# Performance work log

Measured on AMD Instinct MI355X. Metric: run time of the kernel, lower is better.

Reference implementation:

```python
import jax, jax.numpy as jnp
import numpy as np
from jax import lax

B, S, N, F = 64, 512, 30, 1
H, HD = 2, 8              # n_heads, head_dim (gat_hidden=16)
GH = H * HD               # gat_hidden
P = 64                    # projection_dim
LH = 64                   # lstm_hidden
ALPHA = 0.2


def setup_inputs() -> dict:
    key = jax.random.key(0)
    ks = jax.random.split(key, 16)
    x = jax.random.normal(ks[0], (B, S, N, F), dtype=jnp.float32)
    adj = jax.random.randint(ks[1], (N, N), 0, 2).astype(jnp.float32)
    adj = jnp.maximum(adj, jnp.eye(N, dtype=jnp.float32))  # self-loops, no empty rows
    sc = 0.1
    W_gat = sc * jax.random.normal(ks[2], (H, F, HD), dtype=jnp.float32)
    a_src = sc * jax.random.normal(ks[3], (H, HD), dtype=jnp.float32)
    a_dst = sc * jax.random.normal(ks[4], (H, HD), dtype=jnp.float32)
    W_proj = sc * jax.random.normal(ks[5], (N * GH, P), dtype=jnp.float32)
    b_proj = jnp.zeros((P,), dtype=jnp.float32)
    W_ih0 = sc * jax.random.normal(ks[6], (4 * LH, P), dtype=jnp.float32)
    W_hh0 = sc * jax.random.normal(ks[7], (4 * LH, LH), dtype=jnp.float32)
    b_ih0 = jnp.zeros((4 * LH,), dtype=jnp.float32)
    b_hh0 = jnp.zeros((4 * LH,), dtype=jnp.float32)
    W_ih1 = sc * jax.random.normal(ks[8], (4 * LH, LH), dtype=jnp.float32)
    W_hh1 = sc * jax.random.normal(ks[9], (4 * LH, LH), dtype=jnp.float32)
    b_ih1 = jnp.zeros((4 * LH,), dtype=jnp.float32)
    b_hh1 = jnp.zeros((4 * LH,), dtype=jnp.float32)
    W_out = sc * jax.random.normal(ks[10], (LH, N * F), dtype=jnp.float32)
    b_out = jnp.zeros((N * F,), dtype=jnp.float32)
    return dict(x=x, adj=adj, W_gat=W_gat, a_src=a_src, a_dst=a_dst,
                W_proj=W_proj, b_proj=b_proj,
                W_ih0=W_ih0, W_hh0=W_hh0, b_ih0=b_ih0, b_hh0=b_hh0,
                W_ih1=W_ih1, W_hh1=W_hh1, b_ih1=b_ih1, b_hh1=b_hh1,
                W_out=W_out, b_out=b_out)


def _gat(x_flat, adj, W_gat, a_src, a_dst):
    # x_flat: (BS, N, F)
    h = jnp.einsum('bnf,hfd->bhnd', x_flat, W_gat)          # (BS, H, N, HD)
    e_src = jnp.einsum('bhnd,hd->bhn', h, a_src)
    e_dst = jnp.einsum('bhnd,hd->bhn', h, a_dst)
    e = e_src[..., :, None] + e_dst[..., None, :]           # (BS, H, N, N)
    e = jnp.where(e >= 0, e, ALPHA * e)                     # leaky_relu
    e = jnp.where(adj == 0, -jnp.inf, e)
    attn = jax.nn.softmax(e, axis=-1)
    attn = jnp.nan_to_num(attn, nan=0.0)
    out = jnp.einsum('bhij,bhjd->bhid', attn, h)            # (BS, H, N, HD)
    out = jnp.swapaxes(out, 1, 2).reshape(out.shape[0], N, GH)  # head-concat
    out = jnp.where(out > 0, out, jnp.expm1(out))           # elu
    attn_avg = attn.mean(axis=1)                            # (BS, N, N)
    return out, attn_avg


def _lstm_layer(xs, W_ih, W_hh, b_ih, b_hh):
    # xs: (B, S, D) -> (B, S, LH); torch gate order i,f,g,o
    b = xs.shape[0]
    h0 = jnp.zeros((b, LH), xs.dtype)
    c0 = jnp.zeros((b, LH), xs.dtype)

    def step(carry, x_t):
        h, c = carry
        gates = x_t @ W_ih.T + b_ih + h @ W_hh.T + b_hh
        i, f, g, o = jnp.split(gates, 4, axis=-1)
        i, f, o = jax.nn.sigmoid(i), jax.nn.sigmoid(f), jax.nn.sigmoid(o)
        g = jnp.tanh(g)
        c = f * c + i * g
        h = o * jnp.tanh(c)
        return (h, c), h

    (_, _), hs = lax.scan(step, (h0, c0), jnp.swapaxes(xs, 0, 1))
    return jnp.swapaxes(hs, 0, 1)


def reference(x, adj, W_gat, a_src, a_dst, W_proj, b_proj,
              W_ih0, W_hh0, b_ih0, b_hh0, W_ih1, W_hh1, b_ih1, b_hh1,
              W_out, b_out):
    b, s, n, f = x.shape
    x_flat = x.reshape(b * s, n, f)
    gat_out, attn = _gat(x_flat, adj, W_gat, a_src, a_dst)   # (BS,N,GH),(BS,N,N)
    gat_seq = gat_out.reshape(b, s, n * GH)
    gat_seq = jax.nn.relu(gat_seq @ W_proj + b_proj)         # (B,S,P)
    h1 = _lstm_layer(gat_seq, W_ih0, W_hh0, b_ih0, b_hh0)
    h2 = _lstm_layer(h1, W_ih1, W_hh1, b_ih1, b_hh1)
    recon = h2 @ W_out + b_out                               # (B,S,N*F)
    attn_last = attn.reshape(b, s, n, n)[:, -1]              # (B,N,N)
    return recon, attn_last
```

## Files before the change

### kernel.cpp

```cpp
#include <hip/hip_runtime.h>
#include <math.h>

#define BS_TOT 32768
#define NN 30
#define HHD 8
#define GHH 16
#define LHH 64
#define SSS 512
#define BBB 64
#define RECON_SIZE (BBB*SSS*NN)

__device__ __forceinline__ float fsigmoid(float x) {
    return 1.f / (1.f + __expf(-x));
}
__device__ __forceinline__ float ftanh(float x) {
    float ax = fabsf(x);
    float e = __expf(-2.f * ax);
    float r = (1.f - e) / (1.f + e);
    return copysignf(r, x);
}

#define NB 16
__global__ __launch_bounds__(256) void gat_proj_kernel(
    const float* __restrict__ x, const float* __restrict__ adj,
    const float* __restrict__ W_gat, const float* __restrict__ a_src,
    const float* __restrict__ a_dst, const float* __restrict__ W_proj,
    const float* __restrict__ b_proj, float* __restrict__ gat_seq,
    float* __restrict__ attn_out)
{
    __shared__ __align__(16) float gat[NB][480];
    __shared__ __align__(16) float wchunk[96*64];
    __shared__ float x_s[NB][32];
    __shared__ unsigned adjbits[32];

    const int t = threadIdx.x;
    const int bs_base = blockIdx.x * NB;

    for (int rep = 0; rep < 2; ++rep) {
        int idx = rep*256 + t;
        int bl = idx >> 5, j = idx & 31;
        if (j < NN) x_s[bl][j] = x[(bs_base + bl)*NN + j];
    }
    if (t < NN) {
        unsigned bits = 0;
        for (int j = 0; j < NN; ++j)
            if (adj[t*NN + j] != 0.0f) bits |= (1u << j);
        adjbits[t] = bits;
    }
    __syncthreads();

    const int wave = t >> 6, lane = t & 63;
    const int h = lane >> 5, i = lane & 31;
    const bool act = (i < NN);

    float wg[HHD];
    float s_h = 0.f, t_h = 0.f;
    #pragma unroll
    for (int d = 0; d < HHD; ++d) {
        float w = W_gat[h*HHD + d];
        wg[d] = w;
        s_h += w * a_src[h*HHD + d];
        t_h += w * a_dst[h*HHD + d];
    }

    for (int r = 0; r < 4; ++r) {
        const int bl = wave*4 + r;
        const int bs = bs_base + bl;
        const unsigned bits = act ? adjbits[i & 31] : 0u;
        const float xi = act ? x_s[bl][i] : 0.f;
        const float esrc = xi * s_h;

        float m = -1e30f;
        for (int j = 0; j < NN; ++j) {
            if (bits & (1u << j)) {
                float e = esrc + x_s[bl][j] * t_h;
                e = (e >= 0.f) ? e : 0.2f * e;
                m = fmaxf(m, e);
            }
        }
        float Z = 0.f, Sx = 0.f;
        for (int j = 0; j < NN; ++j) {
            if (bits & (1u << j)) {
                float e = esrc + x_s[bl][j] * t_h;
                e = (e >= 0.f) ? e : 0.2f * e;
                float p = expf(e - m);
                Z += p;
                Sx += p * x_s[bl][j];
            }
        }
        const float wsum = Sx / Z;

        if (act) {
            float tmp[8];
            #pragma unroll
            for (int d = 0; d < 8; ++d) {
                float v = wsum * wg[d];
                tmp[d] = (v > 0.f) ? v : expm1f(v);
            }
            float4 v0 = make_float4(tmp[0], tmp[1], tmp[2], tmp[3]);
            float4 v1 = make_float4(tmp[4], tmp[5], tmp[6], tmp[7]);
            *(float4*)&gat[bl][i*GHH + h*HHD]     = v0;
            *(float4*)&gat[bl][i*GHH + h*HHD + 4] = v1;
        }

        if ((bs & (SSS-1)) == (SSS-1)) {
            const int b = bs >> 9;
            for (int j = 0; j < NN; ++j) {
                float a = 0.f;
                if (bits & (1u << j)) {
                    float e = esrc + x_s[bl][j] * t_h;
                    e = (e >= 0.f) ? e : 0.2f * e;
                    a = expf(e - m) / Z;
                }
                float ao = __shfl_xor(a, 32, 64);
                if (act && h == 0)
                    attn_out[b*(NN*NN) + i*NN + j] = 0.5f * (a + ao);
            }
        }
    }
    __syncthreads();

    const int p = t & 63, grp = t >> 6;
    float acc0 = 0.f, acc1 = 0.f, acc2 = 0.f, acc3 = 0.f;
    for (int c = 0; c < 5; ++c) {
        #pragma unroll
        for (int rep = 0; rep < 24; ++rep)
            wchunk[rep*256 + t] = W_proj[c*6144 + rep*256 + t];
        __syncthreads();
        for (int kk = 0; kk < 96; kk += 4) {
            float4 g0 = *(const float4*)&gat[grp*4 + 0][c*96 + kk];
            float4 g1 = *(const float4*)&gat[grp*4 + 1][c*96 + kk];
            float4 g2 = *(const float4*)&gat[grp*4 + 2][c*96 + kk];
            float4 g3 = *(const float4*)&gat[grp*4 + 3][c*96 + kk];
            float w0 = wchunk[(kk+0)*64 + p];
            float w1 = wchunk[(kk+1)*64 + p];
            float w2 = wchunk[(kk+2)*64 + p];
            float w3 = wchunk[(kk+3)*64 + p];
            acc0 += g0.x*w0 + g0.y*w1 + g0.z*w2 + g0.w*w3;
            acc1 += g1.x*w0 + g1.y*w1 + g1.z*w2 + g1.w*w3;
            acc2 += g2.x*w0 + g2.y*w1 + g2.z*w2 + g2.w*w3;
            acc3 += g3.x*w0 + g3.y*w1 + g3.z*w2 + g3.w*w3;
        }
        __syncthreads();
    }
    const float bp = b_proj[p];
    gat_seq[(bs_base + grp*4 + 0)*64 + p] = fmaxf(acc0 + bp, 0.f);
    gat_seq[(bs_base + grp*4 + 1)*64 + p] = fmaxf(acc1 + bp, 0.f);
    gat_seq[(bs_base + grp*4 + 2)*64 + p] = fmaxf(acc2 + bp, 0.f);
    gat_seq[(bs_base + grp*4 + 3)*64 + p] = fmaxf(acc3 + bp, 0.f);
}

__global__ __launch_bounds__(256) void xproj_kernel(
    const float* __restrict__ xin,
    const float* __restrict__ W,
    const float* __restrict__ b_ih, const float* __restrict__ b_hh,
    float* __restrict__ gx)
{
    __shared__ __align__(16) float xt[64][64];
    const int t = threadIdx.x;
    const int r0 = blockIdx.x * 64;

    for (int i = t; i < 64*16; i += 256) {
        int r = i >> 4, c4 = (i & 15) << 2;
        *(float4*)&xt[r][c4] = *(const float4*)&xin[(size_t)(r0 + r)*64 + c4];
    }
    float4 w[16];
    #pragma unroll
    for (int i = 0; i < 16; ++i) w[i] = *(const float4*)&W[t*64 + 4*i];
    const float bias = b_ih[t] + b_hh[t];
    __syncthreads();

    for (int r = 0; r < 64; ++r) {
        float a0 = 0.f, a1 = 0.f, a2 = 0.f, a3 = 0.f;
        #pragma unroll
        for (int i = 0; i < 16; ++i) {
            float4 v = *(const float4*)&xt[r][4*i];
            a0 = fmaf(v.x, w[i].x, a0); a1 = fmaf(v.y, w[i].y, a1);
            a2 = fmaf(v.z, w[i].z, a2); a3 = fmaf(v.w, w[i].w, a3);
        }
        gx[(size_t)(r0 + r)*256 + t] = bias + ((a0 + a1) + (a2 + a3));
    }
}

__global__ __launch_bounds__(1024, 1) void lstm_rec_kernel(
    const float* __restrict__ gx,
    const float* __restrict__ W_hh,
    float* __restrict__ h_out)
{
    __shared__ float h_s[64];
    __shared__ float gates[256];

    const int t = threadIdx.x;
    const int b = blockIdx.x;
    const int row = t >> 2, slice = t & 3;
    const int sect = row >> 6;

    const float4 w0 = *(const float4*)&W_hh[row*64 + slice*16 + 0];
    const float4 w1 = *(const float4*)&W_hh[row*64 + slice*16 + 4];
    const float4 w2 = *(const float4*)&W_hh[row*64 + slice*16 + 8];
    const float4 w3 = *(const float4*)&W_hh[row*64 + slice*16 + 12];

    if (t < 64) h_s[t] = 0.f;
    __syncthreads();

    const float* __restrict__ gxb = gx + (size_t)b * SSS * 256;
    float* __restrict__ hrow = h_out + (size_t)b * SSS * 64;

    float c = 0.f;
    float gx_cur = gxb[row];

    for (int tt = 0; tt < SSS; ++tt) {
        float gx_next = (tt + 1 < SSS) ? gxb[(size_t)(tt+1)*256 + row] : 0.f;

        const float4 h0 = *(const float4*)&h_s[slice*16 + 0];
        const float4 h1 = *(const float4*)&h_s[slice*16 + 4];
        const float4 h2 = *(const float4*)&h_s[slice*16 + 8];
        const float4 h3 = *(const float4*)&h_s[slice*16 + 12];

        float a0 = h0.x*w0.x + h0.y*w0.y + h0.z*w0.z + h0.w*w0.w;
        float a1 = h1.x*w1.x + h1.y*w1.y + h1.z*w1.z + h1.w*w1.w;
        float a2 = h2.x*w2.x + h2.y*w2.y + h2.z*w2.z + h2.w*w2.w;
        float a3 = h3.x*w3.x + h3.y*w3.y + h3.z*w3.z + h3.w*w3.w;
        float acc = (a0 + a1) + (a2 + a3);

        acc += __shfl_xor(acc, 1, 64);
        acc += __shfl_xor(acc, 2, 64);
        acc += gx_cur;

        const float a = (sect == 2) ? ftanh(acc) : fsigmoid(acc);
        if (slice == 0) gates[row] = a;
        __syncthreads();

        if (t < 64) {
            float ig = gates[t], fg = gates[64+t], gg = gates[128+t], og = gates[192+t];
            c = fg*c + ig*gg;
            float hv = og * ftanh(c);
            h_s[t] = hv;
            hrow[(size_t)tt*64 + t] = hv;
        }
        gx_cur = gx_next;
        __syncthreads();
    }
}

__global__ __launch_bounds__(256) void recon_kernel(
    const float* __restrict__ h2, const float* __restrict__ W_out,
    const float* __restrict__ b_out, float* __restrict__ out)
{
    __shared__ __align__(16) float hl[8*64];
    const int t = threadIdx.x;
    const int bs_base = blockIdx.x * 8;

    hl[t]       = h2[(size_t)bs_base*64 + t];
    hl[256 + t] = h2[(size_t)bs_base*64 + 256 + t];
    __syncthreads();

    if (t < 240) {
        const int bl = t / 30;
        const int n  = t - bl*30;
        float acc = b_out[n];
        #pragma unroll
        for (int k = 0; k < 64; ++k)
            acc += hl[bl*64 + k] * W_out[k*NN + n];
        out[(size_t)(bs_base + bl)*NN + n] = acc;
    }
}

extern "C" void kernel_launch(void* const* d_in, const int* in_sizes, int n_in,
                              void* d_out, int out_size, void* d_ws, size_t ws_size,
                              hipStream_t stream)
{
    const float* x      = (const float*)d_in[0];
    const float* adj    = (const float*)d_in[1];
    const float* W_gat  = (const float*)d_in[2];
    const float* a_src  = (const float*)d_in[3];
    const float* a_dst  = (const float*)d_in[4];
    const float* W_proj = (const float*)d_in[5];
    const float* b_proj = (const float*)d_in[6];
    const float* W_ih0  = (const float*)d_in[7];
    const float* W_hh0  = (const float*)d_in[8];
    const float* b_ih0  = (const float*)d_in[9];
    const float* b_hh0  = (const float*)d_in[10];
    const float* W_ih1  = (const float*)d_in[11];
    const float* W_hh1  = (const float*)d_in[12];
    const float* b_ih1  = (const float*)d_in[13];
    const float* b_hh1  = (const float*)d_in[14];
    const float* W_out  = (const float*)d_in[15];
    const float* b_out  = (const float*)d_in[16];

    float* out = (float*)d_out;
    float* gat_seq = (float*)d_ws;
    float* h1  = gat_seq + (size_t)BS_TOT*64;
    float* h2  = h1 + (size_t)BS_TOT*64;
    float* gxb = h2 + (size_t)BS_TOT*64;

    hipLaunchKernelGGL(gat_proj_kernel, dim3(BS_TOT/NB), dim3(256), 0, stream,
                       x, adj, W_gat, a_src, a_dst, W_proj, b_proj,
                       gat_seq, out + RECON_SIZE);
    hipLaunchKernelGGL(xproj_kernel, dim3(BS_TOT/64), dim3(256), 0, stream,
                       gat_seq, W_ih0, b_ih0, b_hh0, gxb);
    hipLaunchKernelGGL(lstm_rec_kernel, dim3(BBB), dim3(1024), 0, stream,
                       gxb, W_hh0, h1);
    hipLaunchKernelGGL(xproj_kernel, dim3(BS_TOT/64), dim3(256), 0, stream,
                       h1, W_ih1, b_ih1, b_hh1, gxb);
    hipLaunchKernelGGL(lstm_rec_kernel, dim3(BBB), dim3(1024), 0, stream,
                       gxb, W_hh1, h2);
    hipLaunchKernelGGL(recon_kernel, dim3(BS_TOT/8), dim3(256), 0, stream,
                       h2, W_out, b_out, out);
}
```

Before: 773.3 us.

## Restructure LSTM recurrence to one barrier per step with wave-local gate exchange

The recurrent LSTM kernel drops from 1024 to 512 threads, so each thread now handles half a weight row (32 elements) instead of a quarter. Threads are arranged so all four gates of a hidden unit sit in the same wavefront and are exchanged with shuffles rather than through shared memory. Double-buffering the hidden state removes one of the two block barriers per timestep. Tanh for the g gate is computed through the sigmoid identity, and the weight registers are pinned with empty asm; the cost is more serial FMAs per thread and more register pressure.

```diff
diff --git a/kernel.cpp b/kernel.cpp
--- a/kernel.cpp
+++ b/kernel.cpp
@@ -182,61 +182,88 @@
     }
 }
 
-__global__ __launch_bounds__(1024, 1) void lstm_rec_kernel(
+__global__ __launch_bounds__(512) void lstm_rec_kernel(
     const float* __restrict__ gx,
     const float* __restrict__ W_hh,
     float* __restrict__ h_out)
 {
-    __shared__ float h_s[64];
-    __shared__ float gates[256];
+    __shared__ __align__(16) float h_s[2][64];
 
     const int t = threadIdx.x;
     const int b = blockIdx.x;
-    const int row = t >> 2, slice = t & 3;
-    const int sect = row >> 6;
-
-    const float4 w0 = *(const float4*)&W_hh[row*64 + slice*16 + 0];
-    const float4 w1 = *(const float4*)&W_hh[row*64 + slice*16 + 4];
-    const float4 w2 = *(const float4*)&W_hh[row*64 + slice*16 + 8];
-    const float4 w3 = *(const float4*)&W_hh[row*64 + slice*16 + 12];
-
-    if (t < 64) h_s[t] = 0.f;
-    __syncthreads();
+    const int lane = t & 63;
+    const int jj = lane >> 3, q = (lane >> 1) & 3, s = lane & 1;
+    const int j = (t >> 6) * 8 + jj;
+    const int row = q * 64 + j;
+    const bool qg = (q == 2);
+    const int gbase = (jj << 3);
+
+    float4 w0 = *(const float4*)&W_hh[row*64 + s*32 +  0];
+    float4 w1 = *(const float4*)&W_hh[row*64 + s*32 +  4];
+    float4 w2 = *(const float4*)&W_hh[row*64 + s*32 +  8];
+    float4 w3 = *(const float4*)&W_hh[row*64 + s*32 + 12];
+    float4 w4 = *(const float4*)&W_hh[row*64 + s*32 + 16];
+    float4 w5 = *(const float4*)&W_hh[row*64 + s*32 + 20];
+    float4 w6 = *(const float4*)&W_hh[row*64 + s*32 + 24];
+    float4 w7 = *(const float4*)&W_hh[row*64 + s*32 + 28];
+#define PIN4(v) asm volatile("" : "+v"(v.x), "+v"(v.y), "+v"(v.z), "+v"(v.w));
+    PIN4(w0) PIN4(w1) PIN4(w2) PIN4(w3) PIN4(w4) PIN4(w5) PIN4(w6) PIN4(w7)
+#undef PIN4
+
+    if (t < 64) { h_s[0][t] = 0.f; }
 
     const float* __restrict__ gxb = gx + (size_t)b * SSS * 256;
     float* __restrict__ hrow = h_out + (size_t)b * SSS * 64;
 
     float c = 0.f;
     float gx_cur = gxb[row];
+    __syncthreads();
 
     for (int tt = 0; tt < SSS; ++tt) {
+        const int cur = tt & 1;
         float gx_next = (tt + 1 < SSS) ? gxb[(size_t)(tt+1)*256 + row] : 0.f;
 
-        const float4 h0 = *(const float4*)&h_s[slice*16 + 0];
-        const float4 h1 = *(const float4*)&h_s[slice*16 + 4];
-        const float4 h2 = *(const float4*)&h_s[slice*16 + 8];
-        const float4 h3 = *(const float4*)&h_s[slice*16 + 12];
+        const float* hb = &h_s[cur][s*32];
+        const float4 h0 = *(const float4*)&hb[0];
+        const float4 h1 = *(const float4*)&hb[4];
+        const float4 h2 = *(const float4*)&hb[8];
+        const float4 h3 = *(const float4*)&hb[12];
+        const float4 h4 = *(const float4*)&hb[16];
+        const float4 h5 = *(const float4*)&hb[20];
+        const float4 h6 = *(const float4*)&hb[24];
+        const float4 h7 = *(const float4*)&hb[28];
 
         float a0 = h0.x*w0.x + h0.y*w0.y + h0.z*w0.z + h0.w*w0.w;
         float a1 = h1.x*w1.x + h1.y*w1.y + h1.z*w1.z + h1.w*w1.w;
         float a2 = h2.x*w2.x + h2.y*w2.y + h2.z*w2.z + h2.w*w2.w;
         float a3 = h3.x*w3.x + h3.y*w3.y + h3.z*w3.z + h3.w*w3.w;
+        a0 = fmaf(h4.x, w4.x, a0); a0 = fmaf(h4.y, w4.y, a0);
+        a0 = fmaf(h4.z, w4.z, a0); a0 = fmaf(h4.w, w4.w, a0);
+        a1 = fmaf(h5.x, w5.x, a1); a1 = fmaf(h5.y, w5.y, a1);
+        a1 = fmaf(h5.z, w5.z, a1); a1 = fmaf(h5.w, w5.w, a1);
+        a2 = fmaf(h6.x, w6.x, a2); a2 = fmaf(h6.y, w6.y, a2);
+        a2 = fmaf(h6.z, w6.z, a2); a2 = fmaf(h6.w, w6.w, a2);
+        a3 = fmaf(h7.x, w7.x, a3); a3 = fmaf(h7.y, w7.y, a3);
+        a3 = fmaf(h7.z, w7.z, a3); a3 = fmaf(h7.w, w7.w, a3);
         float acc = (a0 + a1) + (a2 + a3);
 
         acc += __shfl_xor(acc, 1, 64);
-        acc += __shfl_xor(acc, 2, 64);
         acc += gx_cur;
 
-        const float a = (sect == 2) ? ftanh(acc) : fsigmoid(acc);
-        if (slice == 0) gates[row] = a;
-        __syncthreads();
-
-        if (t < 64) {
-            float ig = gates[t], fg = gates[64+t], gg = gates[128+t], og = gates[192+t];
-            c = fg*c + ig*gg;
-            float hv = og * ftanh(c);
-            h_s[t] = hv;
-            hrow[(size_t)tt*64 + t] = hv;
+        float y = fsigmoid(qg ? 2.f * acc : acc);
+        float act = qg ? fmaf(2.f, y, -1.f) : y;
+
+        float ig = __shfl(act, gbase + 0, 64);
+        float fg = __shfl(act, gbase + 2, 64);
+        float gg = __shfl(act, gbase + 4, 64);
+        float og = __shfl(act, gbase + 6, 64);
+
+        c = fg * c + ig * gg;
+        float hv = og * ftanh(c);
+
+        if ((lane & 7) == 0) {
+            h_s[cur ^ 1][j] = hv;
+            hrow[(size_t)tt*64 + j] = hv;
         }
         gx_cur = gx_next;
         __syncthreads();
@@ -299,11 +326,11 @@
                        gat_seq, out + RECON_SIZE);
     hipLaunchKernelGGL(xproj_kernel, dim3(BS_TOT/64), dim3(256), 0, stream,
                        gat_seq, W_ih0, b_ih0, b_hh0, gxb);
-    hipLaunchKernelGGL(lstm_rec_kernel, dim3(BBB), dim3(1024), 0, stream,
+    hipLaunchKernelGGL(lstm_rec_kernel, dim3(BBB), dim3(512), 0, stream,
                        gxb, W_hh0, h1);
     hipLaunchKernelGGL(xproj_kernel, dim3(BS_TOT/64), dim3(256), 0, stream,
                        h1, W_ih1, b_ih1, b_hh1, gxb);
-    hipLaunchKernelGGL(lstm_rec_kernel, dim3(BBB), dim3(1024), 0, stream,
+    hipLaunchKernelGGL(lstm_rec_kernel, dim3(BBB), dim3(512), 0, stream,
                        gxb, W_hh1, h2);
     hipLaunchKernelGGL(recon_kernel, dim3(BS_TOT/8), dim3(256), 0, stream,
                        h2, W_out, b_out, out);
```

Measured after the change: 800.5 us. 3.5% more time.
